# Kernel optimization log

Measured on AMD Instinct MI355X. Metric: run time of the kernel, lower is better.

The kernel has to match this reference:

```python
import jax, jax.numpy as jnp
import numpy as np

N = 50000
E = 800000
IN_C = 128
HID = 32
OUT_C = 16
NEG_SLOPE = 0.2


def setup_inputs() -> dict:
    key = jax.random.key(0)
    ks = jax.random.split(key, 16)
    x = jax.random.normal(ks[0], (N, IN_C), dtype=jnp.float32)
    edge_index = jax.random.randint(ks[1], (2, E), 0, N, dtype=jnp.int64)

    def glorot(k, shape):
        fan = shape[0] + shape[-1]
        return jax.random.uniform(k, shape, jnp.float32, -1.0, 1.0) * jnp.sqrt(6.0 / fan)

    # layer1: in=128 -> heads=4, ch=32, concat -> out 128
    W1 = glorot(ks[2], (IN_C, 4 * HID))
    a_src1 = glorot(ks[3], (4, HID))
    a_dst1 = glorot(ks[4], (4, HID))
    b1 = jnp.zeros((4 * HID,), jnp.float32)
    # layer2: in=128 -> heads=2, ch=32, concat -> out 64
    W2 = glorot(ks[5], (4 * HID, 2 * HID))
    a_src2 = glorot(ks[6], (2, HID))
    a_dst2 = glorot(ks[7], (2, HID))
    b2 = jnp.zeros((2 * HID,), jnp.float32)
    # layer3: in=64 -> heads=1, ch=16, mean -> out 16
    W3 = glorot(ks[8], (2 * HID, OUT_C))
    a_src3 = glorot(ks[9], (1, OUT_C))
    a_dst3 = glorot(ks[10], (1, OUT_C))
    b3 = jnp.zeros((OUT_C,), jnp.float32)
    return {"x": x, "edge_index": edge_index,
            "W1": W1, "a_src1": a_src1, "a_dst1": a_dst1, "b1": b1,
            "W2": W2, "a_src2": a_src2, "a_dst2": a_dst2, "b2": b2,
            "W3": W3, "a_src3": a_src3, "a_dst3": a_dst3, "b3": b3}


def gat_conv(x, src, dst, W, a_src, a_dst, bias, heads, ch, concat):
    n = x.shape[0]
    h = (x @ W).reshape(n, heads, ch)                      # [N,H,C]
    alpha_s = jnp.einsum('nhc,hc->nh', h, a_src)           # [N,H]
    alpha_d = jnp.einsum('nhc,hc->nh', h, a_dst)           # [N,H]
    logits = jax.nn.leaky_relu(alpha_s[src] + alpha_d[dst], NEG_SLOPE)  # [E,H]
    # segment softmax over edges sharing the same destination node
    m = jax.ops.segment_max(logits, dst, num_segments=n)
    m = jnp.where(jnp.isfinite(m), m, 0.0)
    e = jnp.exp(logits - m[dst])
    denom = jax.ops.segment_sum(e, dst, num_segments=n)
    alpha = e / (denom[dst] + 1e-16)                       # [E,H]
    msg = h[src] * alpha[:, :, None]                       # [E,H,C]
    out = jax.ops.segment_sum(msg, dst, num_segments=n)    # [N,H,C]
    out = out.reshape(n, heads * ch) if concat else out.mean(axis=1)
    return out + bias


def reference(x, edge_index, W1, a_src1, a_dst1, b1, W2, a_src2, a_dst2, b2, W3, a_src3, a_dst3, b3):
    n = x.shape[0]
    loops = jnp.arange(n, dtype=edge_index.dtype)
    src = jnp.concatenate([edge_index[0], loops])  # add self loops (PyG default)
    dst = jnp.concatenate([edge_index[1], loops])
    h = jax.nn.relu(gat_conv(x, src, dst, W1, a_src1, a_dst1, b1, 4, HID, True))
    h = jax.nn.relu(gat_conv(h, src, dst, W2, a_src2, a_dst2, b2, 2, HID, True))
    out = gat_conv(h, src, dst, W3, a_src3, a_dst3, b3, 1, OUT_C, False)
    return out
```

## Files before the change

### kernel.cpp

```cpp
#include <hip/hip_runtime.h>
#include <hip/hip_bf16.h>
#include <stdint.h>

#define NODES 50000
#define NEDGE 800000
#define TEDGE (NEDGE + NODES)
#define SBLK 25
#define HBLK ((TEDGE + 255) / 256)
#define GBLK ((NODES + 63) / 64)

typedef unsigned short u16;
typedef unsigned int u32;
typedef unsigned long long u64;
typedef short s16x8 __attribute__((ext_vector_type(8)));
typedef float f32x4 __attribute__((ext_vector_type(4)));

__device__ __forceinline__ float bf2f(u16 v) {
  return __uint_as_float(((u32)v) << 16);
}
__device__ __forceinline__ u16 f2bf(float f) {
  u32 u = __float_as_uint(f);
  u32 r = (u + 0x7FFFu + ((u >> 16) & 1u)) >> 16;
  return (u16)r;
}
__device__ __forceinline__ float lo16f(u32 w) { return __uint_as_float(w << 16); }
__device__ __forceinline__ float hi16f(u32 w) { return __uint_as_float(w & 0xFFFF0000u); }
__device__ __forceinline__ float lrelu(float x) {
  return (x > 0.f) ? x : 0.2f * x;
}
__device__ __forceinline__ int clampn(int v) {
  return ((u32)v < NODES) ? v : 0;
}
__device__ __forceinline__ float load1(const void* p, size_t i, bool fb) {
  return fb ? bf2f(((const u16*)p)[i]) : ((const float*)p)[i];
}
__device__ __forceinline__ u32 encf(float f) {
  u32 u = __float_as_uint(f);
  return (u & 0x80000000u) ? ~u : (u | 0x80000000u);
}
__device__ __forceinline__ float decf(u32 k) {
  u32 u = (k & 0x80000000u) ? (k & 0x7FFFFFFFu) : ~k;
  return __uint_as_float(u);
}

__global__ __launch_bounds__(256) void k_probe(
    const int* __restrict__ ei, const u16* __restrict__ xs16,
    int* __restrict__ flags, int* __restrict__ deg,
    const void* __restrict__ W1, const void* __restrict__ W2,
    const void* __restrict__ W3, const void* __restrict__ as1,
    const void* __restrict__ ad1, const void* __restrict__ as2,
    const void* __restrict__ ad2, const void* __restrict__ as3,
    const void* __restrict__ ad3, u16* __restrict__ wt1,
    u16* __restrict__ wt2, u16* __restrict__ wt3, u16* __restrict__ wa1,
    u16* __restrict__ wa2, u16* __restrict__ wa3) {
  __shared__ int sfb;
  int t = threadIdx.x;
  int g = blockIdx.x * 256 + t;
  if (g < NODES) deg[g] = 0;
  if (blockIdx.x == 0 && t >= 2 && t < 32) flags[t] = 0;
  if (t < 64) {
    int big = 0;
#pragma unroll
    for (int k = 0; k < 4; ++k) {
      u32 ex = (xs16[2 * (t * 4 + k)] >> 7) & 0xFF;
      big += (ex >= 0x90);
    }
#pragma unroll
    for (int off = 32; off >= 1; off >>= 1) big += __shfl_xor(big, off);
    if (t == 0) sfb = (big >= 8) ? 0 : 1;
    if (blockIdx.x == 0) {
      int odd = 0, even = 0;
#pragma unroll
      for (int k = 0; k < 4; ++k) {
        int idx = t + 64 * k;
        odd |= (ei[2 * idx + 1] != 0);
        even |= (ei[2 * idx] != 0);
      }
      u64 bo = __ballot(odd);
      u64 be = __ballot(even);
      if (t == 0) flags[0] = (bo == 0ull && be != 0ull) ? 1 : 0;
    }
  }
  __syncthreads();
  bool fb = sfb != 0;
  if (blockIdx.x == 0 && t == 0) flags[1] = fb ? 1 : 0;

  auto fidx = [](int n, int k, int KS) {
    int nt = n >> 4, lrow = n & 15, ks = k >> 5, quad = (k >> 3) & 3, j = k & 7;
    return ((size_t)((nt * KS + ks) * 64 + quad * 16 + lrow)) * 8 + j;
  };

  if (g < 16384) {
    int n = g >> 7, k = g & 127;
    wt1[fidx(n, k, 4)] = f2bf(load1(W1, (size_t)k * 128 + n, fb));
  } else if (g < 24576) {
    int r = g - 16384;
    int n = r >> 7, k = r & 127;
    wt2[fidx(n, k, 4)] = f2bf(load1(W2, (size_t)k * 64 + n, fb));
  } else if (g < 25600) {
    int r = g - 24576;
    int n = r >> 6, k = r & 63;
    wt3[fidx(n, k, 2)] = f2bf(load1(W3, (size_t)k * 16 + n, fb));
  } else if (g < 27648) {
    int e = g - 25600;
    int n = e >> 7, k = e & 127;
    float v = 0.f;
    if (n < 8) {
      int head = (n < 4) ? n : n - 4;
      const void* av = (n < 4) ? as1 : ad1;
      for (int c = 0; c < 32; ++c)
        v += load1(W1, (size_t)k * 128 + head * 32 + c, fb) *
             load1(av, head * 32 + c, fb);
    }
    wa1[fidx(n, k, 4)] = (n < 8) ? f2bf(v) : (u16)0;
  } else if (g < 29696) {
    int e = g - 27648;
    int n = e >> 7, k = e & 127;
    float v = 0.f;
    if (n < 4) {
      int head = (n < 2) ? n : n - 2;
      const void* av = (n < 2) ? as2 : ad2;
      for (int c = 0; c < 32; ++c)
        v += load1(W2, (size_t)k * 64 + head * 32 + c, fb) *
             load1(av, head * 32 + c, fb);
    }
    wa2[fidx(n, k, 4)] = (n < 4) ? f2bf(v) : (u16)0;
  } else if (g < 30720) {
    int e = g - 29696;
    int n = e >> 6, k = e & 63;
    float v = 0.f;
    if (n < 2) {
      const void* av = (n < 1) ? as3 : ad3;
      for (int c = 0; c < 16; ++c)
        v += load1(W3, (size_t)k * 16 + c, fb) * load1(av, c, fb);
    }
    wa3[fidx(n, k, 2)] = (n < 2) ? f2bf(v) : (u16)0;
  }
}

template <int K, int N, int H, bool XEXT>
__device__ __forceinline__ void gmfma_tile(const void* __restrict__ xin,
                                           const u16* __restrict__ wtf,
                                           const u16* __restrict__ waf,
                                           u16* __restrict__ hout,
                                           float* __restrict__ asg,
                                           float* __restrict__ adg,
                                           u32* __restrict__ gm,
                                           const int* __restrict__ flags,
                                           int M, int row0,
                                           u16* __restrict__ xlds,
                                           u32* __restrict__ lmax) {
  constexpr int KP = K + 8;
  constexpr int NT = N / 16;
  constexpr int KS = K / 32;
  constexpr int KG = K / 8;
  int t = threadIdx.x;
  bool fb = flags[1] != 0;
  if (t < 2 * H) lmax[t] = 0;

  bool xbf = XEXT ? fb : true;
  for (int i = t; i < 64 * KG; i += 256) {
    int r = i / KG, kg = i % KG;
    int grow = row0 + r;
    if (grow >= M) grow = M - 1;
    if (xbf) {
      *(uint4*)&xlds[r * KP + kg * 8] =
          *(const uint4*)((const u16*)xin + (size_t)grow * K + kg * 8);
    } else {
      const float* gp = (const float*)xin + (size_t)grow * K + kg * 8;
      float4 f0 = *(const float4*)gp, f1 = *(const float4*)(gp + 4);
      *(ushort4*)&xlds[r * KP + kg * 8] =
          make_ushort4(f2bf(f0.x), f2bf(f0.y), f2bf(f0.z), f2bf(f0.w));
      *(ushort4*)&xlds[r * KP + kg * 8 + 4] =
          make_ushort4(f2bf(f1.x), f2bf(f1.y), f2bf(f1.z), f2bf(f1.w));
    }
  }
  __syncthreads();

  int lane = t & 63, w = t >> 6;
  int lrow = lane & 15, quad = lane >> 4;
  f32x4 acc[NT];
  f32x4 eacc = (f32x4){0.f, 0.f, 0.f, 0.f};
#pragma unroll
  for (int nt = 0; nt < NT; ++nt) acc[nt] = (f32x4){0.f, 0.f, 0.f, 0.f};

  const u16* xbase = xlds + (w * 16 + lrow) * KP + quad * 8;
#pragma unroll
  for (int ks = 0; ks < KS; ++ks) {
    s16x8 a = *(const s16x8*)(xbase + ks * 32);
    s16x8 be = *(const s16x8*)(waf + ((size_t)(ks * 64 + lane)) * 8);
    eacc = __builtin_amdgcn_mfma_f32_16x16x32_bf16(a, be, eacc, 0, 0, 0);
#pragma unroll
    for (int nt = 0; nt < NT; ++nt) {
      s16x8 b = *(const s16x8*)(wtf + ((size_t)((nt * KS + ks) * 64 + lane)) * 8);
      acc[nt] = __builtin_amdgcn_mfma_f32_16x16x32_bf16(a, b, acc[nt], 0, 0, 0);
    }
  }

  float pm = -3.4e38f;
  int baserow = row0 + w * 16 + quad * 4;
#pragma unroll
  for (int r = 0; r < 4; ++r) {
    int grow = baserow + r;
    if (grow < M) {
#pragma unroll
      for (int nt = 0; nt < NT; ++nt)
        hout[(size_t)grow * N + nt * 16 + lrow] = f2bf(acc[nt][r]);
      if (lrow < H) asg[grow * H + lrow] = eacc[r];
      else if (lrow < 2 * H) adg[grow * H + (lrow - H)] = eacc[r];
    }
    pm = fmaxf(pm, eacc[r]);
  }
  if (lrow < 2 * H) atomicMax(&lmax[lrow], encf(pm));
  __syncthreads();
  if (t < 2 * H) atomicMax(&gm[t], lmax[t]);
}

template <int K, int N, int H, bool XEXT>
__global__ __launch_bounds__(256) void k_gmfma(const void* __restrict__ xin,
                                               const u16* __restrict__ wtf,
                                               const u16* __restrict__ waf,
                                               u16* __restrict__ hout,
                                               float* __restrict__ asg,
                                               float* __restrict__ adg,
                                               u32* __restrict__ gm,
                                               const int* __restrict__ flags,
                                               int M) {
  __shared__ u16 xlds[64 * (K + 8)];
  __shared__ u32 lmax[2 * H];
  gmfma_tile<K, N, H, XEXT>(xin, wtf, waf, hout, asg, adg, gm, flags, M,
                            blockIdx.x * 64, xlds, lmax);
}

__global__ __launch_bounds__(256) void k_build_l1(
    const void* __restrict__ xin, const u16* __restrict__ wtf,
    const u16* __restrict__ waf, u16* __restrict__ hout,
    float* __restrict__ asg, float* __restrict__ adg, u32* __restrict__ gm,
    const int* __restrict__ flags, const int* __restrict__ ei,
    int* __restrict__ deg, u16* __restrict__ rankarr,
    u16* __restrict__ src16, u16* __restrict__ dst16) {
  __shared__ u16 xlds[64 * 136];
  __shared__ u32 lmax[8];
  int bi = blockIdx.x;
  if (bi < HBLK) {
    int e = bi * 256 + threadIdx.x;
    if (e >= TEDGE) return;
    int d, s;
    if (e < NEDGE) {
      if (flags[0]) { s = ei[2 * e]; d = ei[2 * (NEDGE + e)]; }
      else { s = ei[e]; d = ei[NEDGE + e]; }
    } else {
      s = e - NEDGE; d = s;
    }
    s = clampn(s); d = clampn(d);
    src16[e] = (u16)s;
    dst16[e] = (u16)d;
    int r = atomicAdd(&deg[d], 1);
    rankarr[e] = (u16)min(r, 65535);
    return;
  }
  gmfma_tile<128, 128, 4, true>(xin, wtf, waf, hout, asg, adg, gm, flags,
                                NODES, (bi - HBLK) * 64, xlds, lmax);
}

__global__ __launch_bounds__(1024) void k_scan(const int* __restrict__ deg,
                                               int* __restrict__ rowptr,
                                               int* __restrict__ parts,
                                               int* __restrict__ counter) {
  __shared__ int swave[16];
  __shared__ int sbase, stot;
  int b = blockIdx.x, t = threadIdx.x;
  int lane = t & 63, w = t >> 6;
  int i0 = b * 2048 + t * 2;
  int v0 = (i0 < NODES) ? deg[i0] : 0;
  int v1 = (i0 + 1 < NODES) ? deg[i0 + 1] : 0;
  int local = v0 + v1;
  int x = local;
#pragma unroll
  for (int off = 1; off < 64; off <<= 1) {
    int y = __shfl_up(x, off);
    if (lane >= off) x += y;
  }
  if (lane == 63) swave[w] = x;
  __syncthreads();
  if (w == 0) {
    int wv = (lane < 16) ? swave[lane] : 0;
#pragma unroll
    for (int off = 1; off < 16; off <<= 1) {
      int y = __shfl_up(wv, off);
      if (lane >= off) wv += y;
    }
    if (lane == 15) {
      __hip_atomic_store(&parts[b], wv, __ATOMIC_RELAXED,
                         __HIP_MEMORY_SCOPE_AGENT);
      __hip_atomic_fetch_add(counter, 1, __ATOMIC_RELEASE,
                             __HIP_MEMORY_SCOPE_AGENT);
    }
    if (lane < 16) swave[lane] = wv;
  }
  __syncthreads();
  if (t == 0) {
    while (__hip_atomic_load(counter, __ATOMIC_ACQUIRE,
                             __HIP_MEMORY_SCOPE_AGENT) < SBLK)
      __builtin_amdgcn_s_sleep(2);
  }
  __syncthreads();
  if (w == 0) {
    int pv = (lane < SBLK) ? __hip_atomic_load(&parts[lane], __ATOMIC_RELAXED,
                                               __HIP_MEMORY_SCOPE_AGENT)
                           : 0;
    int pb = (lane < b) ? pv : 0;
#pragma unroll
    for (int off = 32; off >= 1; off >>= 1) {
      pb += __shfl_xor(pb, off);
      pv += __shfl_xor(pv, off);
    }
    if (lane == 0) { sbase = pb; stot = pv; }
  }
  __syncthreads();
  int run = sbase + ((w == 0) ? 0 : swave[w - 1]) + (x - local);
  if (i0 < NODES) rowptr[i0] = run;
  if (i0 + 1 < NODES) rowptr[i0 + 1] = run + v0;
  if (b == 0 && t == 0) rowptr[NODES] = stot;
}

__global__ __launch_bounds__(256) void k_scatter(const u16* __restrict__ src16,
                                                 const u16* __restrict__ dst16,
                                                 const int* __restrict__ rowptr,
                                                 const u16* __restrict__ rankarr,
                                                 u16* __restrict__ srcs) {
  int e = blockIdx.x * 256 + threadIdx.x;
  if (e >= TEDGE) return;
  int d = dst16[e];
  int pos = rowptr[d] + (int)rankarr[e];
  srcs[pos] = src16[e];
}

template <int H, int C, bool RELU, bool FINAL>
__global__ __launch_bounds__(256) void k_agg(const u16* __restrict__ hbuf,
                                             const float* __restrict__ asg,
                                             const float* __restrict__ adg,
                                             const int* __restrict__ rowptr,
                                             const u16* __restrict__ srcs,
                                             const void* __restrict__ bias,
                                             const int* __restrict__ flags,
                                             const u32* __restrict__ gm,
                                             void* __restrict__ outp, int n) {
  constexpr int HC = H * C;
  constexpr int L = HC / 8;
  constexpr int EPN = 32 / L;
  constexpr int UN = (4 * EPN <= 32) ? 4 : 2;
  __shared__ u16 lds_s[4][64];
  __shared__ float lds_e[4][64][H];
  int lane = threadIdx.x & 63;
  int w = threadIdx.x >> 6;
  int nh = lane >> 5;
  int hl = lane & 31;
  int node = blockIdx.x * 8 + w * 2 + nh;
  if (node >= n) node = n - 1;
  bool fb = flags[1] != 0;
  int start = rowptr[node], end = rowptr[node + 1];
  if (end < start || end - start > TEDGE) { start = 0; end = 0; }

  float adh[H], M[H];
#pragma unroll
  for (int h = 0; h < H; ++h) adh[h] = adg[node * H + h];
#pragma unroll
  for (int h = 0; h < H; ++h) M[h] = lrelu(decf(gm[h]) + decf(gm[H + h]));

  int sub = hl / L;
  int cl = hl & (L - 1);
  int ch0 = cl * 8;
  int myhead = ch0 / C;
  int base = nh * 32;

  float den[H];
#pragma unroll
  for (int h = 0; h < H; ++h) den[h] = 0.f;
  float acc[UN][8];
#pragma unroll
  for (int u = 0; u < UN; ++u)
#pragma unroll
    for (int i = 0; i < 8; ++i) acc[u][i] = 0.f;

  for (int chunk = start; chunk < end; chunk += 32) {
    int e = chunk + hl;
    int s = 0;
    float ee[H];
#pragma unroll
    for (int h = 0; h < H; ++h) ee[h] = 0.f;
    if (e < end) {
      s = srcs[e];
      float av[H];
      if (H == 4) { float4 t4 = *(const float4*)(asg + s * 4);
        av[0] = t4.x; av[1] = t4.y; av[H > 2 ? 2 : 0] = t4.z; av[H > 3 ? 3 : 0] = t4.w; }
      else if (H == 2) { float2 t2 = *(const float2*)(asg + s * 2); av[0] = t2.x; av[1] = t2.y; }
      else av[0] = asg[s];
#pragma unroll
      for (int h = 0; h < H; ++h) {
        float x = __expf(lrelu(av[h] + adh[h]) - M[h]);
        ee[h] = x;
        den[h] += x;
      }
    }
    __builtin_amdgcn_wave_barrier();
    lds_s[w][lane] = (u16)s;
#pragma unroll
    for (int h = 0; h < H; ++h) lds_e[w][lane][h] = ee[h];
    __builtin_amdgcn_wave_barrier();

    int cn = min(32, end - chunk);
    for (int j = 0; j < cn; j += UN * EPN) {
      int sx[UN];
      float ax[UN];
#pragma unroll
      for (int u = 0; u < UN; ++u) {
        int ei_ = base + j + u * EPN + sub;
        sx[u] = lds_s[w][ei_];
        ax[u] = lds_e[w][ei_][myhead];
      }
#pragma unroll
      for (int u = 0; u < UN; ++u) {
        uint4 v = *(const uint4*)(hbuf + (size_t)sx[u] * HC + ch0);
        acc[u][0] += ax[u] * lo16f(v.x); acc[u][1] += ax[u] * hi16f(v.x);
        acc[u][2] += ax[u] * lo16f(v.y); acc[u][3] += ax[u] * hi16f(v.y);
        acc[u][4] += ax[u] * lo16f(v.z); acc[u][5] += ax[u] * hi16f(v.z);
        acc[u][6] += ax[u] * lo16f(v.w); acc[u][7] += ax[u] * hi16f(v.w);
      }
    }
  }

#pragma unroll
  for (int m = 16; m >= 1; m >>= 1) {
#pragma unroll
    for (int h = 0; h < H; ++h) den[h] += __shfl_xor(den[h], m);
  }
  float tt[8];
#pragma unroll
  for (int i = 0; i < 8; ++i) {
    tt[i] = acc[0][i];
#pragma unroll
    for (int u = 1; u < UN; ++u) tt[i] += acc[u][i];
  }
#pragma unroll
  for (int m = L; m < 32; m <<= 1) {
#pragma unroll
    for (int i = 0; i < 8; ++i) tt[i] += __shfl_xor(tt[i], m);
  }

  if (sub == 0) {
    float inv = 1.f / (den[myhead] + 1e-16f);
    float o[8];
#pragma unroll
    for (int i = 0; i < 8; ++i) {
      o[i] = tt[i] * inv + load1(bias, ch0 + i, fb);
      if (RELU) o[i] = fmaxf(o[i], 0.f);
    }
    bool obf = FINAL ? fb : true;
    if (obf) {
      uint4 pk;
      pk.x = (u32)f2bf(o[0]) | ((u32)f2bf(o[1]) << 16);
      pk.y = (u32)f2bf(o[2]) | ((u32)f2bf(o[3]) << 16);
      pk.z = (u32)f2bf(o[4]) | ((u32)f2bf(o[5]) << 16);
      pk.w = (u32)f2bf(o[6]) | ((u32)f2bf(o[7]) << 16);
      *(uint4*)((u16*)outp + (size_t)node * HC + ch0) = pk;
    } else {
      float* op = (float*)outp + (size_t)node * HC + ch0;
      *(float4*)op = make_float4(o[0], o[1], o[2], o[3]);
      *(float4*)(op + 4) = make_float4(o[4], o[5], o[6], o[7]);
    }
  }
}


extern "C" void kernel_launch(void* const* d_in, const int* in_sizes, int n_in,
                              void* d_out, int out_size, void* d_ws, size_t ws_size,
                              hipStream_t stream) {
  const void* x   = d_in[0];
  const int* ei   = (const int*)d_in[1];
  const void* W1  = d_in[2];
  const void* as1 = d_in[3];
  const void* ad1 = d_in[4];
  const void* b1  = d_in[5];
  const void* W2  = d_in[6];
  const void* as2 = d_in[7];
  const void* ad2 = d_in[8];
  const void* b2  = d_in[9];
  const void* W3  = d_in[10];
  const void* as3 = d_in[11];
  const void* ad3 = d_in[12];
  const void* b3  = d_in[13];

  char* w = (char*)d_ws;
  auto alloc = [&](size_t bytes) {
    char* p = w;
    w += (bytes + 255) & ~(size_t)255;
    return p;
  };
  int* flags    = (int*)alloc(256);
  int* parts    = (int*)alloc(256);
  int* deg      = (int*)alloc((size_t)NODES * 4);
  int* rowptr   = (int*)alloc((size_t)(NODES + 1) * 4);
  u16* rankarr  = (u16*)alloc((size_t)TEDGE * 2);
  u16* src16    = (u16*)alloc((size_t)TEDGE * 2);
  u16* dst16    = (u16*)alloc((size_t)TEDGE * 2);
  u16* srcs     = (u16*)alloc((size_t)TEDGE * 2);
  float* asg    = (float*)alloc((size_t)NODES * 4 * 4);
  float* adg    = (float*)alloc((size_t)NODES * 4 * 4);
  u16* wt1      = (u16*)alloc((size_t)128 * 128 * 2);
  u16* wt2      = (u16*)alloc((size_t)64 * 128 * 2);
  u16* wt3      = (u16*)alloc((size_t)16 * 64 * 2);
  u16* wa1      = (u16*)alloc((size_t)16 * 128 * 2);
  u16* wa2      = (u16*)alloc((size_t)16 * 128 * 2);
  u16* wa3      = (u16*)alloc((size_t)16 * 64 * 2);
  u16* hbuf     = (u16*)alloc((size_t)NODES * 128 * 2);
  u16* obuf     = (u16*)alloc((size_t)NODES * 128 * 2);

  u32* gm1 = (u32*)(flags + 8);
  u32* gm2 = (u32*)(flags + 16);
  u32* gm3 = (u32*)(flags + 24);

  int ablocks = (NODES + 7) / 8;

  k_probe<<<(NODES + 255) / 256, 256, 0, stream>>>(
      ei, (const u16*)x, flags, deg, W1, W2, W3, as1, ad1, as2, ad2, as3, ad3,
      wt1, wt2, wt3, wa1, wa2, wa3);
  k_build_l1<<<HBLK + GBLK, 256, 0, stream>>>(x, wt1, wa1, hbuf, asg, adg,
                                              gm1, flags, ei, deg, rankarr,
                                              src16, dst16);
  k_scan<<<SBLK, 1024, 0, stream>>>(deg, rowptr, parts, flags + 2);
  k_scatter<<<(TEDGE + 255) / 256, 256, 0, stream>>>(src16, dst16, rowptr, rankarr, srcs);

  k_agg<4, 32, true, false><<<ablocks, 256, 0, stream>>>(hbuf, asg, adg, rowptr, srcs, b1, flags, gm1, obuf, NODES);
  k_gmfma<128, 64, 2, false><<<GBLK, 256, 0, stream>>>(obuf, wt2, wa2, hbuf, asg, adg, gm2, flags, NODES);
  k_agg<2, 32, true, false><<<ablocks, 256, 0, stream>>>(hbuf, asg, adg, rowptr, srcs, b2, flags, gm2, obuf, NODES);
  k_gmfma<64, 16, 1, false><<<GBLK, 256, 0, stream>>>(obuf, wt3, wa3, hbuf, asg, adg, gm3, flags, NODES);
  k_agg<1, 16, false, true><<<ablocks, 256, 0, stream>>>(hbuf, asg, adg, rowptr, srcs, b3, flags, gm3, d_out, NODES);
}
```

Baseline: 268.8 us.

## Interleave edge-build and GEMM blocks, batch atomics, pack src/dst into one word

The combined build kernel now interleaves edge-processing blocks with GEMM tiles (one edge block per two GEMM blocks), so both kinds of work run concurrently rather than in separate phases. Each edge block now covers 8 edges per thread and issues its degree atomics in a batch for more memory-level parallelism. Source and destination are packed into a single u32 array, and the scatter kernel handles 4 edges per thread, which cuts separate loads and the number of blocks launched. The costs are higher register pressure in the edge path and a grid layout that depends on the exact block count ratio.

Measured after the change: 267.4 us. Within noise of the previous version (-0.5%).

```diff
diff --git a/kernel.cpp b/kernel.cpp
--- a/kernel.cpp
+++ b/kernel.cpp
@@ -6,8 +6,9 @@
 #define NEDGE 800000
 #define TEDGE (NEDGE + NODES)
 #define SBLK 25
-#define HBLK ((TEDGE + 255) / 256)
 #define GBLK ((NODES + 63) / 64)
+#define HBLK8 ((TEDGE + 2047) / 2048)
+#define BL1_TOT (3 * HBLK8)
 
 typedef unsigned short u16;
 typedef unsigned int u32;
@@ -238,29 +239,51 @@
     float* __restrict__ asg, float* __restrict__ adg, u32* __restrict__ gm,
     const int* __restrict__ flags, const int* __restrict__ ei,
     int* __restrict__ deg, u16* __restrict__ rankarr,
-    u16* __restrict__ src16, u16* __restrict__ dst16) {
+    u32* __restrict__ sd) {
   __shared__ u16 xlds[64 * 136];
   __shared__ u32 lmax[8];
   int bi = blockIdx.x;
-  if (bi < HBLK) {
-    int e = bi * 256 + threadIdx.x;
-    if (e >= TEDGE) return;
-    int d, s;
-    if (e < NEDGE) {
-      if (flags[0]) { s = ei[2 * e]; d = ei[2 * (NEDGE + e)]; }
-      else { s = ei[e]; d = ei[NEDGE + e]; }
-    } else {
-      s = e - NEDGE; d = s;
-    }
-    s = clampn(s); d = clampn(d);
-    src16[e] = (u16)s;
-    dst16[e] = (u16)d;
-    int r = atomicAdd(&deg[d], 1);
-    rankarr[e] = (u16)min(r, 65535);
+  int r3 = bi % 3;
+  if (r3 == 2) {
+    int hb = bi / 3;
+    int base = hb * 2048 + threadIdx.x;
+    bool odd = flags[0] != 0;
+    int sv[8], dv[8];
+#pragma unroll
+    for (int u = 0; u < 8; ++u) {
+      int e = base + u * 256;
+      int s = 0, d = 0;
+      if (e < TEDGE) {
+        if (e < NEDGE) {
+          if (odd) { s = ei[2 * e]; d = ei[2 * (NEDGE + e)]; }
+          else { s = ei[e]; d = ei[NEDGE + e]; }
+        } else {
+          s = e - NEDGE; d = s;
+        }
+        s = clampn(s); d = clampn(d);
+      }
+      sv[u] = s; dv[u] = d;
+    }
+    int rk[8];
+#pragma unroll
+    for (int u = 0; u < 8; ++u) {
+      int e = base + u * 256;
+      rk[u] = (e < TEDGE) ? atomicAdd(&deg[dv[u]], 1) : 0;
+    }
+#pragma unroll
+    for (int u = 0; u < 8; ++u) {
+      int e = base + u * 256;
+      if (e < TEDGE) {
+        sd[e] = (u32)sv[u] | ((u32)dv[u] << 16);
+        rankarr[e] = (u16)min(rk[u], 65535);
+      }
+    }
     return;
   }
+  int gb = (bi / 3) * 2 + r3;
+  if (gb >= GBLK) return;
   gmfma_tile<128, 128, 4, true>(xin, wtf, waf, hout, asg, adg, gm, flags,
-                                NODES, (bi - HBLK) * 64, xlds, lmax);
+                                NODES, gb * 64, xlds, lmax);
 }
 
 __global__ __launch_bounds__(1024) void k_scan(const int* __restrict__ deg,
@@ -324,16 +347,20 @@
   if (b == 0 && t == 0) rowptr[NODES] = stot;
 }
 
-__global__ __launch_bounds__(256) void k_scatter(const u16* __restrict__ src16,
-                                                 const u16* __restrict__ dst16,
+__global__ __launch_bounds__(256) void k_scatter(const u32* __restrict__ sd,
                                                  const int* __restrict__ rowptr,
                                                  const u16* __restrict__ rankarr,
                                                  u16* __restrict__ srcs) {
-  int e = blockIdx.x * 256 + threadIdx.x;
-  if (e >= TEDGE) return;
-  int d = dst16[e];
-  int pos = rowptr[d] + (int)rankarr[e];
-  srcs[pos] = src16[e];
+  int base = blockIdx.x * 1024 + threadIdx.x;
+#pragma unroll
+  for (int u = 0; u < 4; ++u) {
+    int e = base + u * 256;
+    if (e < TEDGE) {
+      u32 v = sd[e];
+      int pos = rowptr[v >> 16] + (int)rankarr[e];
+      srcs[pos] = (u16)(v & 0xFFFFu);
+    }
+  }
 }
 
 template <int H, int C, bool RELU, bool FINAL>
@@ -502,8 +529,7 @@
   int* deg      = (int*)alloc((size_t)NODES * 4);
   int* rowptr   = (int*)alloc((size_t)(NODES + 1) * 4);
   u16* rankarr  = (u16*)alloc((size_t)TEDGE * 2);
-  u16* src16    = (u16*)alloc((size_t)TEDGE * 2);
-  u16* dst16    = (u16*)alloc((size_t)TEDGE * 2);
+  u32* sd       = (u32*)alloc((size_t)TEDGE * 4);
   u16* srcs     = (u16*)alloc((size_t)TEDGE * 2);
   float* asg    = (float*)alloc((size_t)NODES * 4 * 4);
   float* adg    = (float*)alloc((size_t)NODES * 4 * 4);
@@ -525,11 +551,10 @@
   k_probe<<<(NODES + 255) / 256, 256, 0, stream>>>(
       ei, (const u16*)x, flags, deg, W1, W2, W3, as1, ad1, as2, ad2, as3, ad3,
       wt1, wt2, wt3, wa1, wa2, wa3);
-  k_build_l1<<<HBLK + GBLK, 256, 0, stream>>>(x, wt1, wa1, hbuf, asg, adg,
-                                              gm1, flags, ei, deg, rankarr,
-                                              src16, dst16);
+  k_build_l1<<<BL1_TOT, 256, 0, stream>>>(x, wt1, wa1, hbuf, asg, adg, gm1,
+                                          flags, ei, deg, rankarr, sd);
   k_scan<<<SBLK, 1024, 0, stream>>>(deg, rowptr, parts, flags + 2);
-  k_scatter<<<(TEDGE + 255) / 256, 256, 0, stream>>>(src16, dst16, rowptr, rankarr, srcs);
+  k_scatter<<<(TEDGE + 1023) / 1024, 256, 0, stream>>>(sd, rowptr, rankarr, srcs);
 
   k_agg<4, 32, true, false><<<ablocks, 256, 0, stream>>>(hbuf, asg, adg, rowptr, srcs, b1, flags, gm1, obuf, NODES);
   k_gmfma<128, 64, 2, false><<<GBLK, 256, 0, stream>>>(obuf, wt2, wa2, hbuf, asg, adg, gm2, flags, NODES);
```

## Build CSR in one persistent kernel with LDS histograms and grid barriers

Applied to the files above, without the earlier changes.

Replaces the global-atomic degree count, separate scan kernel and scatter kernel with a single 64-block persistent kernel. Each block builds a 16-bit packed LDS histogram over its edge chunk, publishes per-block counts, then uses grid-wide spin barriers to compute per-node prefix offsets and the row pointer scan before scattering sources from registers. It also splits the fused layer-1 matmul back out into its own launch. The aim is fewer global atomics, fewer launches and no intermediate edge arrays. The cost is only 64 blocks doing the edge work, extra cnt/basecnt traffic, and reliance on all blocks being co-resident for the spin barriers.

After: 278.8 us. 3.7% more time.

```diff
diff --git a/kernel.cpp b/kernel.cpp
--- a/kernel.cpp
+++ b/kernel.cpp
@@ -5,9 +5,11 @@
 #define NODES 50000
 #define NEDGE 800000
 #define TEDGE (NEDGE + NODES)
-#define SBLK 25
-#define HBLK ((TEDGE + 255) / 256)
 #define GBLK ((NODES + 63) / 64)
+#define CSRB 64
+#define CSRCH 13312
+#define NRB 784
+#define NRN 50176
 
 typedef unsigned short u16;
 typedef unsigned int u32;
@@ -45,7 +47,7 @@
 
 __global__ __launch_bounds__(256) void k_probe(
     const int* __restrict__ ei, const u16* __restrict__ xs16,
-    int* __restrict__ flags, int* __restrict__ deg,
+    int* __restrict__ flags,
     const void* __restrict__ W1, const void* __restrict__ W2,
     const void* __restrict__ W3, const void* __restrict__ as1,
     const void* __restrict__ ad1, const void* __restrict__ as2,
@@ -56,7 +58,6 @@
   __shared__ int sfb;
   int t = threadIdx.x;
   int g = blockIdx.x * 256 + t;
-  if (g < NODES) deg[g] = 0;
   if (blockIdx.x == 0 && t >= 2 && t < 32) flags[t] = 0;
   if (t < 64) {
     int big = 0;
@@ -138,23 +139,153 @@
   }
 }
 
+__global__ __launch_bounds__(1024) void k_csr(const int* __restrict__ ei,
+                                              const int* __restrict__ flags,
+                                              u16* __restrict__ cnt,
+                                              u16* __restrict__ basecnt,
+                                              int* __restrict__ rowptr,
+                                              int* __restrict__ parts,
+                                              int* __restrict__ ctrs,
+                                              u16* __restrict__ srcs) {
+  __shared__ u32 hcnt[NRN / 2];
+  __shared__ int swave[16];
+  __shared__ int sbase, stot;
+  int b = blockIdx.x, t = threadIdx.x;
+
+  for (int i = t; i < NRN / 2; i += 1024) hcnt[i] = 0;
+  __syncthreads();
+  bool odd = flags[0] != 0;
+  int ebase = b * CSRCH;
+  int sv[13], dv[13], rk[13];
+#pragma unroll
+  for (int i = 0; i < 13; ++i) {
+    int e = ebase + i * 1024 + t;
+    int s = 0, d = 0, r = -1;
+    if (e < TEDGE) {
+      if (e < NEDGE) {
+        if (odd) { s = ei[2 * e]; d = ei[2 * (NEDGE + e)]; }
+        else { s = ei[e]; d = ei[NEDGE + e]; }
+      } else {
+        s = e - NEDGE; d = s;
+      }
+      s = clampn(s); d = clampn(d);
+      u32 old = atomicAdd(&hcnt[d >> 1], 1u << (16 * (d & 1)));
+      r = (int)((old >> (16 * (d & 1))) & 0xFFFFu);
+    }
+    sv[i] = s; dv[i] = d; rk[i] = r;
+  }
+  __syncthreads();
+  {
+    u32* crow = (u32*)(cnt + (size_t)b * NRN);
+    for (int i = t; i < NRN / 2; i += 1024) crow[i] = hcnt[i];
+  }
+  __syncthreads();
+  if (t == 0) {
+    __hip_atomic_fetch_add(&ctrs[0], 1, __ATOMIC_RELEASE,
+                           __HIP_MEMORY_SCOPE_AGENT);
+    while (__hip_atomic_load(&ctrs[0], __ATOMIC_ACQUIRE,
+                             __HIP_MEMORY_SCOPE_AGENT) < CSRB)
+      __builtin_amdgcn_s_sleep(2);
+  }
+  __syncthreads();
+
+  int dg = 0;
+  int d0 = b * NRB + t;
+  if (t < NRB && d0 < NODES) {
+    int acc = 0;
+    for (int s = 0; s < CSRB; ++s) {
+      u16 c = cnt[(size_t)s * NRN + d0];
+      basecnt[(size_t)s * NRN + d0] = (u16)acc;
+      acc += c;
+    }
+    dg = acc;
+  }
+  int lane = t & 63, w = t >> 6;
+  int x = dg;
+#pragma unroll
+  for (int off = 1; off < 64; off <<= 1) {
+    int y = __shfl_up(x, off);
+    if (lane >= off) x += y;
+  }
+  if (lane == 63) swave[w] = x;
+  __syncthreads();
+  if (w == 0) {
+    int wv = (lane < 16) ? swave[lane] : 0;
+#pragma unroll
+    for (int off = 1; off < 16; off <<= 1) {
+      int y = __shfl_up(wv, off);
+      if (lane >= off) wv += y;
+    }
+    if (lane == 15) {
+      __hip_atomic_store(&parts[b], wv, __ATOMIC_RELAXED,
+                         __HIP_MEMORY_SCOPE_AGENT);
+      __hip_atomic_fetch_add(&ctrs[1], 1, __ATOMIC_RELEASE,
+                             __HIP_MEMORY_SCOPE_AGENT);
+    }
+    if (lane < 16) swave[lane] = wv;
+  }
+  __syncthreads();
+  if (t == 0) {
+    while (__hip_atomic_load(&ctrs[1], __ATOMIC_ACQUIRE,
+                             __HIP_MEMORY_SCOPE_AGENT) < CSRB)
+      __builtin_amdgcn_s_sleep(2);
+  }
+  __syncthreads();
+  if (w == 0) {
+    int pv = (lane < CSRB) ? __hip_atomic_load(&parts[lane], __ATOMIC_RELAXED,
+                                               __HIP_MEMORY_SCOPE_AGENT)
+                           : 0;
+    int pb = (lane < b) ? pv : 0;
+#pragma unroll
+    for (int off = 32; off >= 1; off >>= 1) {
+      pb += __shfl_xor(pb, off);
+      pv += __shfl_xor(pv, off);
+    }
+    if (lane == 0) { sbase = pb; stot = pv; }
+  }
+  __syncthreads();
+  int excl = sbase + ((w == 0) ? 0 : swave[w - 1]) + (x - dg);
+  if (t < NRB && d0 < NODES) rowptr[d0] = excl;
+  if (b == 0 && t == 0) rowptr[NODES] = stot;
+  __syncthreads();
+  if (t == 0) {
+    __hip_atomic_fetch_add(&ctrs[2], 1, __ATOMIC_RELEASE,
+                           __HIP_MEMORY_SCOPE_AGENT);
+    while (__hip_atomic_load(&ctrs[2], __ATOMIC_ACQUIRE,
+                             __HIP_MEMORY_SCOPE_AGENT) < CSRB)
+      __builtin_amdgcn_s_sleep(2);
+  }
+  __syncthreads();
+
+#pragma unroll
+  for (int i = 0; i < 13; ++i) {
+    int e = ebase + i * 1024 + t;
+    if (e < TEDGE) {
+      int d = dv[i];
+      int pos = rowptr[d] + (int)basecnt[(size_t)b * NRN + d] + rk[i];
+      srcs[pos] = (u16)sv[i];
+    }
+  }
+}
+
 template <int K, int N, int H, bool XEXT>
-__device__ __forceinline__ void gmfma_tile(const void* __restrict__ xin,
-                                           const u16* __restrict__ wtf,
-                                           const u16* __restrict__ waf,
-                                           u16* __restrict__ hout,
-                                           float* __restrict__ asg,
-                                           float* __restrict__ adg,
-                                           u32* __restrict__ gm,
-                                           const int* __restrict__ flags,
-                                           int M, int row0,
-                                           u16* __restrict__ xlds,
-                                           u32* __restrict__ lmax) {
+__global__ __launch_bounds__(256) void k_gmfma(const void* __restrict__ xin,
+                                               const u16* __restrict__ wtf,
+                                               const u16* __restrict__ waf,
+                                               u16* __restrict__ hout,
+                                               float* __restrict__ asg,
+                                               float* __restrict__ adg,
+                                               u32* __restrict__ gm,
+                                               const int* __restrict__ flags,
+                                               int M) {
   constexpr int KP = K + 8;
   constexpr int NT = N / 16;
   constexpr int KS = K / 32;
   constexpr int KG = K / 8;
+  __shared__ u16 xlds[64 * KP];
+  __shared__ u32 lmax[2 * H];
   int t = threadIdx.x;
+  int row0 = blockIdx.x * 64;
   bool fb = flags[1] != 0;
   if (t < 2 * H) lmax[t] = 0;
 
@@ -214,126 +345,6 @@
   if (lrow < 2 * H) atomicMax(&lmax[lrow], encf(pm));
   __syncthreads();
   if (t < 2 * H) atomicMax(&gm[t], lmax[t]);
-}
-
-template <int K, int N, int H, bool XEXT>
-__global__ __launch_bounds__(256) void k_gmfma(const void* __restrict__ xin,
-                                               const u16* __restrict__ wtf,
-                                               const u16* __restrict__ waf,
-                                               u16* __restrict__ hout,
-                                               float* __restrict__ asg,
-                                               float* __restrict__ adg,
-                                               u32* __restrict__ gm,
-                                               const int* __restrict__ flags,
-                                               int M) {
-  __shared__ u16 xlds[64 * (K + 8)];
-  __shared__ u32 lmax[2 * H];
-  gmfma_tile<K, N, H, XEXT>(xin, wtf, waf, hout, asg, adg, gm, flags, M,
-                            blockIdx.x * 64, xlds, lmax);
-}
-
-__global__ __launch_bounds__(256) void k_build_l1(
-    const void* __restrict__ xin, const u16* __restrict__ wtf,
-    const u16* __restrict__ waf, u16* __restrict__ hout,
-    float* __restrict__ asg, float* __restrict__ adg, u32* __restrict__ gm,
-    const int* __restrict__ flags, const int* __restrict__ ei,
-    int* __restrict__ deg, u16* __restrict__ rankarr,
-    u16* __restrict__ src16, u16* __restrict__ dst16) {
-  __shared__ u16 xlds[64 * 136];
-  __shared__ u32 lmax[8];
-  int bi = blockIdx.x;
-  if (bi < HBLK) {
-    int e = bi * 256 + threadIdx.x;
-    if (e >= TEDGE) return;
-    int d, s;
-    if (e < NEDGE) {
-      if (flags[0]) { s = ei[2 * e]; d = ei[2 * (NEDGE + e)]; }
-      else { s = ei[e]; d = ei[NEDGE + e]; }
-    } else {
-      s = e - NEDGE; d = s;
-    }
-    s = clampn(s); d = clampn(d);
-    src16[e] = (u16)s;
-    dst16[e] = (u16)d;
-    int r = atomicAdd(&deg[d], 1);
-    rankarr[e] = (u16)min(r, 65535);
-    return;
-  }
-  gmfma_tile<128, 128, 4, true>(xin, wtf, waf, hout, asg, adg, gm, flags,
-                                NODES, (bi - HBLK) * 64, xlds, lmax);
-}
-
-__global__ __launch_bounds__(1024) void k_scan(const int* __restrict__ deg,
-                                               int* __restrict__ rowptr,
-                                               int* __restrict__ parts,
-                                               int* __restrict__ counter) {
-  __shared__ int swave[16];
-  __shared__ int sbase, stot;
-  int b = blockIdx.x, t = threadIdx.x;
-  int lane = t & 63, w = t >> 6;
-  int i0 = b * 2048 + t * 2;
-  int v0 = (i0 < NODES) ? deg[i0] : 0;
-  int v1 = (i0 + 1 < NODES) ? deg[i0 + 1] : 0;
-  int local = v0 + v1;
-  int x = local;
-#pragma unroll
-  for (int off = 1; off < 64; off <<= 1) {
-    int y = __shfl_up(x, off);
-    if (lane >= off) x += y;
-  }
-  if (lane == 63) swave[w] = x;
-  __syncthreads();
-  if (w == 0) {
-    int wv = (lane < 16) ? swave[lane] : 0;
-#pragma unroll
-    for (int off = 1; off < 16; off <<= 1) {
-      int y = __shfl_up(wv, off);
-      if (lane >= off) wv += y;
-    }
-    if (lane == 15) {
-      __hip_atomic_store(&parts[b], wv, __ATOMIC_RELAXED,
-                         __HIP_MEMORY_SCOPE_AGENT);
-      __hip_atomic_fetch_add(counter, 1, __ATOMIC_RELEASE,
-                             __HIP_MEMORY_SCOPE_AGENT);
-    }
-    if (lane < 16) swave[lane] = wv;
-  }
-  __syncthreads();
-  if (t == 0) {
-    while (__hip_atomic_load(counter, __ATOMIC_ACQUIRE,
-                             __HIP_MEMORY_SCOPE_AGENT) < SBLK)
-      __builtin_amdgcn_s_sleep(2);
-  }
-  __syncthreads();
-  if (w == 0) {
-    int pv = (lane < SBLK) ? __hip_atomic_load(&parts[lane], __ATOMIC_RELAXED,
-                                               __HIP_MEMORY_SCOPE_AGENT)
-                           : 0;
-    int pb = (lane < b) ? pv : 0;
-#pragma unroll
-    for (int off = 32; off >= 1; off >>= 1) {
-      pb += __shfl_xor(pb, off);
-      pv += __shfl_xor(pv, off);
-    }
-    if (lane == 0) { sbase = pb; stot = pv; }
-  }
-  __syncthreads();
-  int run = sbase + ((w == 0) ? 0 : swave[w - 1]) + (x - local);
-  if (i0 < NODES) rowptr[i0] = run;
-  if (i0 + 1 < NODES) rowptr[i0 + 1] = run + v0;
-  if (b == 0 && t == 0) rowptr[NODES] = stot;
-}
-
-__global__ __launch_bounds__(256) void k_scatter(const u16* __restrict__ src16,
-                                                 const u16* __restrict__ dst16,
-                                                 const int* __restrict__ rowptr,
-                                                 const u16* __restrict__ rankarr,
-                                                 u16* __restrict__ srcs) {
-  int e = blockIdx.x * 256 + threadIdx.x;
-  if (e >= TEDGE) return;
-  int d = dst16[e];
-  int pos = rowptr[d] + (int)rankarr[e];
-  srcs[pos] = src16[e];
 }
 
 template <int H, int C, bool RELU, bool FINAL>
@@ -499,11 +510,9 @@
   };
   int* flags    = (int*)alloc(256);
   int* parts    = (int*)alloc(256);
-  int* deg      = (int*)alloc((size_t)NODES * 4);
   int* rowptr   = (int*)alloc((size_t)(NODES + 1) * 4);
-  u16* rankarr  = (u16*)alloc((size_t)TEDGE * 2);
-  u16* src16    = (u16*)alloc((size_t)TEDGE * 2);
-  u16* dst16    = (u16*)alloc((size_t)TEDGE * 2);
+  u16* cnt      = (u16*)alloc((size_t)CSRB * NRN * 2);
+  u16* basecnt  = (u16*)alloc((size_t)CSRB * NRN * 2);
   u16* srcs     = (u16*)alloc((size_t)TEDGE * 2);
   float* asg    = (float*)alloc((size_t)NODES * 4 * 4);
   float* adg    = (float*)alloc((size_t)NODES * 4 * 4);
@@ -523,14 +532,11 @@
   int ablocks = (NODES + 7) / 8;
 
   k_probe<<<(NODES + 255) / 256, 256, 0, stream>>>(
-      ei, (const u16*)x, flags, deg, W1, W2, W3, as1, ad1, as2, ad2, as3, ad3,
+      ei, (const u16*)x, flags, W1, W2, W3, as1, ad1, as2, ad2, as3, ad3,
       wt1, wt2, wt3, wa1, wa2, wa3);
-  k_build_l1<<<HBLK + GBLK, 256, 0, stream>>>(x, wt1, wa1, hbuf, asg, adg,
-                                              gm1, flags, ei, deg, rankarr,
-                                              src16, dst16);
-  k_scan<<<SBLK, 1024, 0, stream>>>(deg, rowptr, parts, flags + 2);
-  k_scatter<<<(TEDGE + 255) / 256, 256, 0, stream>>>(src16, dst16, rowptr, rankarr, srcs);
-
+  k_csr<<<CSRB, 1024, 0, stream>>>(ei, flags, cnt, basecnt, rowptr, parts,
+                                   flags + 2, srcs);
+  k_gmfma<128, 128, 4, true><<<GBLK, 256, 0, stream>>>(x, wt1, wa1, hbuf, asg, adg, gm1, flags, NODES);
   k_agg<4, 32, true, false><<<ablocks, 256, 0, stream>>>(hbuf, asg, adg, rowptr, srcs, b1, flags, gm1, obuf, NODES);
   k_gmfma<128, 64, 2, false><<<GBLK, 256, 0, stream>>>(obuf, wt2, wa2, hbuf, asg, adg, gm2, flags, NODES);
   k_agg<2, 32, true, false><<<ablocks, 256, 0, stream>>>(hbuf, asg, adg, rowptr, srcs, b2, flags, gm2, obuf, NODES);
```

## Build CSR with LDS-privatized chunked histograms instead of global atomics

Applied to the files above, without the earlier changes.

Replaces global atomicAdd degree counting with per-chunk shared-memory histograms. Each block handles one chunk of edges and one half of the node range, using packed 16-bit counters in LDS. A new fold kernel prefix-sums the per-chunk counts into per-chunk bases and degrees, and the scatter uses rowptr plus chunk base plus local rank. This removes contended global atomics, but it splits the layer-1 matmul out of the fused build kernel into a separate launch and adds a fold pass over a 64 x 50k count matrix.

Result: no change. 265.4 us (-1.3%).

```diff
diff --git a/kernel.cpp b/kernel.cpp
--- a/kernel.cpp
+++ b/kernel.cpp
@@ -6,8 +6,11 @@
 #define NEDGE 800000
 #define TEDGE (NEDGE + NODES)
 #define SBLK 25
-#define HBLK ((TEDGE + 255) / 256)
 #define GBLK ((NODES + 63) / 64)
+#define CHNK 64
+#define CSRCH 13312
+#define HALFN 25088
+#define NSTR (2 * HALFN)
 
 typedef unsigned short u16;
 typedef unsigned int u32;
@@ -45,7 +48,7 @@
 
 __global__ __launch_bounds__(256) void k_probe(
     const int* __restrict__ ei, const u16* __restrict__ xs16,
-    int* __restrict__ flags, int* __restrict__ deg,
+    int* __restrict__ flags,
     const void* __restrict__ W1, const void* __restrict__ W2,
     const void* __restrict__ W3, const void* __restrict__ as1,
     const void* __restrict__ ad1, const void* __restrict__ as2,
@@ -56,7 +59,6 @@
   __shared__ int sfb;
   int t = threadIdx.x;
   int g = blockIdx.x * 256 + t;
-  if (g < NODES) deg[g] = 0;
   if (blockIdx.x == 0 && t >= 2 && t < 32) flags[t] = 0;
   if (t < 64) {
     int big = 0;
@@ -138,23 +140,154 @@
   }
 }
 
+__global__ __launch_bounds__(1024) void k_hista(const int* __restrict__ ei,
+                                                const int* __restrict__ flags,
+                                                u32* __restrict__ sd,
+                                                u16* __restrict__ rank16,
+                                                u16* __restrict__ cnt) {
+  __shared__ u32 hcnt[HALFN / 2];
+  int b = blockIdx.x;
+  int c = b >> 1, half = b & 1;
+  int t = threadIdx.x;
+  for (int i = t; i < HALFN / 2; i += 1024) hcnt[i] = 0;
+  __syncthreads();
+  bool odd = flags[0] != 0;
+  int ebase = c * CSRCH;
+  int nlo = half * HALFN;
+#pragma unroll
+  for (int i = 0; i < 13; ++i) {
+    int e = ebase + i * 1024 + t;
+    if (e < TEDGE) {
+      int s, d;
+      if (e < NEDGE) {
+        if (odd) { s = ei[2 * e]; d = ei[2 * (NEDGE + e)]; }
+        else { s = ei[e]; d = ei[NEDGE + e]; }
+      } else {
+        s = e - NEDGE; d = s;
+      }
+      s = clampn(s); d = clampn(d);
+      if (half == 0) sd[e] = (u32)s | ((u32)d << 16);
+      int li = d - nlo;
+      if ((u32)li < HALFN) {
+        u32 old = atomicAdd(&hcnt[li >> 1], 1u << (16 * (li & 1)));
+        rank16[e] = (u16)((old >> (16 * (li & 1))) & 0xFFFFu);
+      }
+    }
+  }
+  __syncthreads();
+  u32* crow = (u32*)(cnt + (size_t)c * NSTR + nlo);
+  for (int i = t; i < HALFN / 2; i += 1024) crow[i] = hcnt[i];
+}
+
+__global__ __launch_bounds__(256) void k_fold(const u16* __restrict__ cnt,
+                                              u16* __restrict__ basecnt,
+                                              int* __restrict__ deg) {
+  int n = blockIdx.x * 256 + threadIdx.x;
+  if (n >= NODES) return;
+  int acc = 0;
+#pragma unroll 8
+  for (int c = 0; c < CHNK; ++c) {
+    u16 v = cnt[(size_t)c * NSTR + n];
+    basecnt[(size_t)c * NSTR + n] = (u16)acc;
+    acc += v;
+  }
+  deg[n] = acc;
+}
+
+__global__ __launch_bounds__(1024) void k_scan(const int* __restrict__ deg,
+                                               int* __restrict__ rowptr,
+                                               int* __restrict__ parts,
+                                               int* __restrict__ counter) {
+  __shared__ int swave[16];
+  __shared__ int sbase, stot;
+  int b = blockIdx.x, t = threadIdx.x;
+  int lane = t & 63, w = t >> 6;
+  int i0 = b * 2048 + t * 2;
+  int v0 = (i0 < NODES) ? deg[i0] : 0;
+  int v1 = (i0 + 1 < NODES) ? deg[i0 + 1] : 0;
+  int local = v0 + v1;
+  int x = local;
+#pragma unroll
+  for (int off = 1; off < 64; off <<= 1) {
+    int y = __shfl_up(x, off);
+    if (lane >= off) x += y;
+  }
+  if (lane == 63) swave[w] = x;
+  __syncthreads();
+  if (w == 0) {
+    int wv = (lane < 16) ? swave[lane] : 0;
+#pragma unroll
+    for (int off = 1; off < 16; off <<= 1) {
+      int y = __shfl_up(wv, off);
+      if (lane >= off) wv += y;
+    }
+    if (lane == 15) {
+      __hip_atomic_store(&parts[b], wv, __ATOMIC_RELAXED,
+                         __HIP_MEMORY_SCOPE_AGENT);
+      __hip_atomic_fetch_add(counter, 1, __ATOMIC_RELEASE,
+                             __HIP_MEMORY_SCOPE_AGENT);
+    }
+    if (lane < 16) swave[lane] = wv;
+  }
+  __syncthreads();
+  if (t == 0) {
+    while (__hip_atomic_load(counter, __ATOMIC_ACQUIRE,
+                             __HIP_MEMORY_SCOPE_AGENT) < SBLK)
+      __builtin_amdgcn_s_sleep(2);
+  }
+  __syncthreads();
+  if (w == 0) {
+    int pv = (lane < SBLK) ? __hip_atomic_load(&parts[lane], __ATOMIC_RELAXED,
+                                               __HIP_MEMORY_SCOPE_AGENT)
+                           : 0;
+    int pb = (lane < b) ? pv : 0;
+#pragma unroll
+    for (int off = 32; off >= 1; off >>= 1) {
+      pb += __shfl_xor(pb, off);
+      pv += __shfl_xor(pv, off);
+    }
+    if (lane == 0) { sbase = pb; stot = pv; }
+  }
+  __syncthreads();
+  int run = sbase + ((w == 0) ? 0 : swave[w - 1]) + (x - local);
+  if (i0 < NODES) rowptr[i0] = run;
+  if (i0 + 1 < NODES) rowptr[i0 + 1] = run + v0;
+  if (b == 0 && t == 0) rowptr[NODES] = stot;
+}
+
+__global__ __launch_bounds__(1024) void k_scatter(const u32* __restrict__ sd,
+                                                  const u16* __restrict__ rank16,
+                                                  const u16* __restrict__ basecnt,
+                                                  const int* __restrict__ rowptr,
+                                                  u16* __restrict__ srcs) {
+  int c = blockIdx.x / 13;
+  int r = blockIdx.x % 13;
+  int e = c * CSRCH + r * 1024 + threadIdx.x;
+  if (e >= TEDGE) return;
+  u32 v = sd[e];
+  int d = (int)(v >> 16);
+  int pos = rowptr[d] + (int)basecnt[(size_t)c * NSTR + d] + (int)rank16[e];
+  srcs[pos] = (u16)(v & 0xFFFFu);
+}
+
 template <int K, int N, int H, bool XEXT>
-__device__ __forceinline__ void gmfma_tile(const void* __restrict__ xin,
-                                           const u16* __restrict__ wtf,
-                                           const u16* __restrict__ waf,
-                                           u16* __restrict__ hout,
-                                           float* __restrict__ asg,
-                                           float* __restrict__ adg,
-                                           u32* __restrict__ gm,
-                                           const int* __restrict__ flags,
-                                           int M, int row0,
-                                           u16* __restrict__ xlds,
-                                           u32* __restrict__ lmax) {
+__global__ __launch_bounds__(256) void k_gmfma(const void* __restrict__ xin,
+                                               const u16* __restrict__ wtf,
+                                               const u16* __restrict__ waf,
+                                               u16* __restrict__ hout,
+                                               float* __restrict__ asg,
+                                               float* __restrict__ adg,
+                                               u32* __restrict__ gm,
+                                               const int* __restrict__ flags,
+                                               int M) {
   constexpr int KP = K + 8;
   constexpr int NT = N / 16;
   constexpr int KS = K / 32;
   constexpr int KG = K / 8;
+  __shared__ u16 xlds[64 * KP];
+  __shared__ u32 lmax[2 * H];
   int t = threadIdx.x;
+  int row0 = blockIdx.x * 64;
   bool fb = flags[1] != 0;
   if (t < 2 * H) lmax[t] = 0;
 
@@ -214,126 +347,6 @@
   if (lrow < 2 * H) atomicMax(&lmax[lrow], encf(pm));
   __syncthreads();
   if (t < 2 * H) atomicMax(&gm[t], lmax[t]);
-}
-
-template <int K, int N, int H, bool XEXT>
-__global__ __launch_bounds__(256) void k_gmfma(const void* __restrict__ xin,
-                                               const u16* __restrict__ wtf,
-                                               const u16* __restrict__ waf,
-                                               u16* __restrict__ hout,
-                                               float* __restrict__ asg,
-                                               float* __restrict__ adg,
-                                               u32* __restrict__ gm,
-                                               const int* __restrict__ flags,
-                                               int M) {
-  __shared__ u16 xlds[64 * (K + 8)];
-  __shared__ u32 lmax[2 * H];
-  gmfma_tile<K, N, H, XEXT>(xin, wtf, waf, hout, asg, adg, gm, flags, M,
-                            blockIdx.x * 64, xlds, lmax);
-}
-
-__global__ __launch_bounds__(256) void k_build_l1(
-    const void* __restrict__ xin, const u16* __restrict__ wtf,
-    const u16* __restrict__ waf, u16* __restrict__ hout,
-    float* __restrict__ asg, float* __restrict__ adg, u32* __restrict__ gm,
-    const int* __restrict__ flags, const int* __restrict__ ei,
-    int* __restrict__ deg, u16* __restrict__ rankarr,
-    u16* __restrict__ src16, u16* __restrict__ dst16) {
-  __shared__ u16 xlds[64 * 136];
-  __shared__ u32 lmax[8];
-  int bi = blockIdx.x;
-  if (bi < HBLK) {
-    int e = bi * 256 + threadIdx.x;
-    if (e >= TEDGE) return;
-    int d, s;
-    if (e < NEDGE) {
-      if (flags[0]) { s = ei[2 * e]; d = ei[2 * (NEDGE + e)]; }
-      else { s = ei[e]; d = ei[NEDGE + e]; }
-    } else {
-      s = e - NEDGE; d = s;
-    }
-    s = clampn(s); d = clampn(d);
-    src16[e] = (u16)s;
-    dst16[e] = (u16)d;
-    int r = atomicAdd(&deg[d], 1);
-    rankarr[e] = (u16)min(r, 65535);
-    return;
-  }
-  gmfma_tile<128, 128, 4, true>(xin, wtf, waf, hout, asg, adg, gm, flags,
-                                NODES, (bi - HBLK) * 64, xlds, lmax);
-}
-
-__global__ __launch_bounds__(1024) void k_scan(const int* __restrict__ deg,
-                                               int* __restrict__ rowptr,
-                                               int* __restrict__ parts,
-                                               int* __restrict__ counter) {
-  __shared__ int swave[16];
-  __shared__ int sbase, stot;
-  int b = blockIdx.x, t = threadIdx.x;
-  int lane = t & 63, w = t >> 6;
-  int i0 = b * 2048 + t * 2;
-  int v0 = (i0 < NODES) ? deg[i0] : 0;
-  int v1 = (i0 + 1 < NODES) ? deg[i0 + 1] : 0;
-  int local = v0 + v1;
-  int x = local;
-#pragma unroll
-  for (int off = 1; off < 64; off <<= 1) {
-    int y = __shfl_up(x, off);
-    if (lane >= off) x += y;
-  }
-  if (lane == 63) swave[w] = x;
-  __syncthreads();
-  if (w == 0) {
-    int wv = (lane < 16) ? swave[lane] : 0;
-#pragma unroll
-    for (int off = 1; off < 16; off <<= 1) {
-      int y = __shfl_up(wv, off);
-      if (lane >= off) wv += y;
-    }
-    if (lane == 15) {
-      __hip_atomic_store(&parts[b], wv, __ATOMIC_RELAXED,
-                         __HIP_MEMORY_SCOPE_AGENT);
-      __hip_atomic_fetch_add(counter, 1, __ATOMIC_RELEASE,
-                             __HIP_MEMORY_SCOPE_AGENT);
-    }
-    if (lane < 16) swave[lane] = wv;
-  }
-  __syncthreads();
-  if (t == 0) {
-    while (__hip_atomic_load(counter, __ATOMIC_ACQUIRE,
-                             __HIP_MEMORY_SCOPE_AGENT) < SBLK)
-      __builtin_amdgcn_s_sleep(2);
-  }
-  __syncthreads();
-  if (w == 0) {
-    int pv = (lane < SBLK) ? __hip_atomic_load(&parts[lane], __ATOMIC_RELAXED,
-                                               __HIP_MEMORY_SCOPE_AGENT)
-                           : 0;
-    int pb = (lane < b) ? pv : 0;
-#pragma unroll
-    for (int off = 32; off >= 1; off >>= 1) {
-      pb += __shfl_xor(pb, off);
-      pv += __shfl_xor(pv, off);
-    }
-    if (lane == 0) { sbase = pb; stot = pv; }
-  }
-  __syncthreads();
-  int run = sbase + ((w == 0) ? 0 : swave[w - 1]) + (x - local);
-  if (i0 < NODES) rowptr[i0] = run;
-  if (i0 + 1 < NODES) rowptr[i0 + 1] = run + v0;
-  if (b == 0 && t == 0) rowptr[NODES] = stot;
-}
-
-__global__ __launch_bounds__(256) void k_scatter(const u16* __restrict__ src16,
-                                                 const u16* __restrict__ dst16,
-                                                 const int* __restrict__ rowptr,
-                                                 const u16* __restrict__ rankarr,
-                                                 u16* __restrict__ srcs) {
-  int e = blockIdx.x * 256 + threadIdx.x;
-  if (e >= TEDGE) return;
-  int d = dst16[e];
-  int pos = rowptr[d] + (int)rankarr[e];
-  srcs[pos] = src16[e];
 }
 
 template <int H, int C, bool RELU, bool FINAL>
@@ -501,9 +514,10 @@
   int* parts    = (int*)alloc(256);
   int* deg      = (int*)alloc((size_t)NODES * 4);
   int* rowptr   = (int*)alloc((size_t)(NODES + 1) * 4);
-  u16* rankarr  = (u16*)alloc((size_t)TEDGE * 2);
-  u16* src16    = (u16*)alloc((size_t)TEDGE * 2);
-  u16* dst16    = (u16*)alloc((size_t)TEDGE * 2);
+  u16* cnt      = (u16*)alloc((size_t)CHNK * NSTR * 2);
+  u16* basecnt  = (u16*)alloc((size_t)CHNK * NSTR * 2);
+  u32* sd       = (u32*)alloc((size_t)TEDGE * 4);
+  u16* rank16   = (u16*)alloc((size_t)TEDGE * 2);
   u16* srcs     = (u16*)alloc((size_t)TEDGE * 2);
   float* asg    = (float*)alloc((size_t)NODES * 4 * 4);
   float* adg    = (float*)alloc((size_t)NODES * 4 * 4);
@@ -523,14 +537,14 @@
   int ablocks = (NODES + 7) / 8;
 
   k_probe<<<(NODES + 255) / 256, 256, 0, stream>>>(
-      ei, (const u16*)x, flags, deg, W1, W2, W3, as1, ad1, as2, ad2, as3, ad3,
+      ei, (const u16*)x, flags, W1, W2, W3, as1, ad1, as2, ad2, as3, ad3,
       wt1, wt2, wt3, wa1, wa2, wa3);
-  k_build_l1<<<HBLK + GBLK, 256, 0, stream>>>(x, wt1, wa1, hbuf, asg, adg,
-                                              gm1, flags, ei, deg, rankarr,
-                                              src16, dst16);
+  k_hista<<<2 * CHNK, 1024, 0, stream>>>(ei, flags, sd, rank16, cnt);
+  k_fold<<<(NODES + 255) / 256, 256, 0, stream>>>(cnt, basecnt, deg);
   k_scan<<<SBLK, 1024, 0, stream>>>(deg, rowptr, parts, flags + 2);
-  k_scatter<<<(TEDGE + 255) / 256, 256, 0, stream>>>(src16, dst16, rowptr, rankarr, srcs);
-
+  k_scatter<<<CHNK * 13, 1024, 0, stream>>>(sd, rank16, basecnt, rowptr, srcs);
+
+  k_gmfma<128, 128, 4, true><<<GBLK, 256, 0, stream>>>(x, wt1, wa1, hbuf, asg, adg, gm1, flags, NODES);
   k_agg<4, 32, true, false><<<ablocks, 256, 0, stream>>>(hbuf, asg, adg, rowptr, srcs, b1, flags, gm1, obuf, NODES);
   k_gmfma<128, 64, 2, false><<<GBLK, 256, 0, stream>>>(obuf, wt2, wa2, hbuf, asg, adg, gm2, flags, NODES);
   k_agg<2, 32, true, false><<<ablocks, 256, 0, stream>>>(hbuf, asg, adg, rowptr, srcs, b2, flags, gm2, obuf, NODES);
```
